# Performance work log

Measured on AMD Instinct MI355X. Metric: run time of the kernel, lower is better.

Reference implementation:

```python
import jax, jax.numpy as jnp
import numpy as np

NUM_HEADS = 32
NUM_KV_HEADS = 8  # num_heads // 4 (GQA)
HEAD_DIM = 64     # hidden_size // num_heads
ROPE_BASE = 10000.0


def _rotate_half(x):
    x1, x2 = jnp.split(x, 2, axis=-1)
    return jnp.concatenate((-x2, x1), axis=-1)


def _rope_cos_sin(seq_len, dtype):
    inv_freq = 1.0 / (ROPE_BASE ** (jnp.arange(0, HEAD_DIM, 2, dtype=jnp.float32) / HEAD_DIM))
    t = jnp.arange(seq_len, dtype=jnp.float32)
    freqs = jnp.outer(t, inv_freq)                 # [S, HEAD_DIM//2]
    emb = jnp.concatenate((freqs, freqs), axis=-1) # [S, HEAD_DIM]
    return jnp.cos(emb).astype(dtype), jnp.sin(emb).astype(dtype)


def setup_inputs() -> dict:
    key = jax.random.key(0)
    ks = jax.random.split(key, 5)
    B, S, H = 1, 2048, 2048
    KV = NUM_KV_HEADS * HEAD_DIM  # 512
    s = 0.02
    return {
        "hidden_states": jax.random.normal(ks[0], (B, S, H), jnp.float32),
        "Wq": jax.random.normal(ks[1], (H, H), jnp.float32) * s,
        "Wk": jax.random.normal(ks[2], (KV, H), jnp.float32) * s,
        "Wv": jax.random.normal(ks[3], (KV, H), jnp.float32) * s,
        "Wo": jax.random.normal(ks[4], (H, H), jnp.float32) * s,
    }


def reference(hidden_states, Wq, Wk, Wv, Wo):
    B, S, H = hidden_states.shape
    dtype = hidden_states.dtype
    # QKV projections (nn.Linear with weight [out,in], no bias)
    q = jnp.einsum("bsh,oh->bso", hidden_states, Wq)
    k = jnp.einsum("bsh,oh->bso", hidden_states, Wk)
    v = jnp.einsum("bsh,oh->bso", hidden_states, Wv)
    q = q.reshape(B, S, NUM_HEADS, HEAD_DIM).transpose(0, 2, 1, 3)      # [B,H,S,D]
    k = k.reshape(B, S, NUM_KV_HEADS, HEAD_DIM).transpose(0, 2, 1, 3)   # [B,KV,S,D]
    v = v.reshape(B, S, NUM_KV_HEADS, HEAD_DIM).transpose(0, 2, 1, 3)
    # RoPE
    cos, sin = _rope_cos_sin(S, dtype)  # [S,D] broadcast over batch/heads
    q = q * cos + _rotate_half(q) * sin
    k = k * cos + _rotate_half(k) * sin
    # GQA: repeat_interleave KV heads
    groups = NUM_HEADS // NUM_KV_HEADS
    k = jnp.repeat(k, groups, axis=1)
    v = jnp.repeat(v, groups, axis=1)
    # Attention: scores in fp32 softmax, causal mask (additive)
    scale = 1.0 / np.sqrt(HEAD_DIM)
    scores = jnp.einsum("bhqd,bhkd->bhqk", q, k) * scale
    causal = jnp.tril(jnp.ones((S, S), dtype=bool))
    scores = jnp.where(causal, scores, jnp.finfo(jnp.float32).min)
    probs = jax.nn.softmax(scores.astype(jnp.float32), axis=-1).astype(dtype)
    attn = jnp.einsum("bhqk,bhkd->bhqd", probs, v)
    attn = attn.transpose(0, 2, 1, 3).reshape(B, S, H)
    return jnp.einsum("bsh,oh->bso", attn, Wo)
```

## Files before the change

### kernel.cpp

```cpp
#include <hip/hip_runtime.h>
#include <hip/hip_bf16.h>
#include <math.h>

typedef __hip_bfloat16 bf16;
typedef __attribute__((ext_vector_type(8))) short short8;
typedef __attribute__((ext_vector_type(4))) short short4v;
typedef __attribute__((ext_vector_type(4))) float floatx4;

#define MFMA16(a, b, c) __builtin_amdgcn_mfma_f32_16x16x32_bf16((a), (b), (c), 0, 0, 0)

typedef const __attribute__((address_space(1))) void* as1_cvp;
typedef __attribute__((address_space(3))) void* as3_vp;

__device__ __forceinline__ void gload_lds16(const bf16* g, bf16* lds_uni) {
    __builtin_amdgcn_global_load_lds((as1_cvp)g, (as3_vp)lds_uni, 16, 0, 0);
}

__global__ __launch_bounds__(256) void cvt_all(
    const float* __restrict__ a0, const float* __restrict__ a1,
    const float* __restrict__ a2, const float* __restrict__ a3,
    const float* __restrict__ a4,
    bf16* __restrict__ d0, bf16* __restrict__ d1, bf16* __restrict__ d2,
    bf16* __restrict__ d3, bf16* __restrict__ d4)
{
    const int b = blockIdx.x;
    const float* src; bf16* dst; int off;
    if (b < 2048)      { src = a0; dst = d0; off = b; }
    else if (b < 4096) { src = a1; dst = d1; off = b - 2048; }
    else if (b < 4608) { src = a2; dst = d2; off = b - 4096; }
    else if (b < 5120) { src = a3; dst = d3; off = b - 4608; }
    else               { src = a4; dst = d4; off = b - 5120; }
    const int i = (off * 256 + threadIdx.x) * 8;
    const float4 x = *(const float4*)(src + i);
    const float4 y = *(const float4*)(src + i + 4);
    bf16 t[8];
    t[0] = __float2bfloat16(x.x); t[1] = __float2bfloat16(x.y);
    t[2] = __float2bfloat16(x.z); t[3] = __float2bfloat16(x.w);
    t[4] = __float2bfloat16(y.x); t[5] = __float2bfloat16(y.y);
    t[6] = __float2bfloat16(y.z); t[7] = __float2bfloat16(y.w);
    *(short8*)(dst + i) = *(const short8*)t;
}

#define GEMM_K_LOOP_12864(KB)                                                   \
    for (int k0 = 0; k0 < (KB); k0 += 64) {                                     \
        gload_lds16(gA + k0,            ldsA);                                  \
        gload_lds16(gA + A64 + k0,      ldsA + 2048);                           \
        gload_lds16(gB + k0,            ldsB);                                  \
        gload_lds16(gA + k0 + 32,       ldsA + 4096);                           \
        gload_lds16(gA + A64 + k0 + 32, ldsA + 6144);                           \
        gload_lds16(gB + k0 + 32,       ldsB + 2048);                           \
        __syncthreads();                                                        \
        _Pragma("unroll")                                                       \
        for (int hh = 0; hh < 2; ++hh) {                                        \
            short8 af[2], bfr[4];                                               \
            _Pragma("unroll")                                                   \
            for (int i = 0; i < 2; ++i)                                         \
                af[i] = *(const short8*)&As[hh * 4096 + (w * 32 + i * 16 + l15) * 32 + quad * 8]; \
            _Pragma("unroll")                                                   \
            for (int j = 0; j < 4; ++j)                                         \
                bfr[j] = *(const short8*)&Bs[hh * 2048 + (j * 16 + l15) * 32 + quad * 8]; \
            _Pragma("unroll")                                                   \
            for (int i = 0; i < 2; ++i)                                         \
                _Pragma("unroll")                                               \
                for (int j = 0; j < 4; ++j)                                     \
                    acc[i][j] = MFMA16(af[i], bfr[j], acc[i][j]);               \
        }                                                                       \
        __syncthreads();                                                        \
    }

__global__ __launch_bounds__(256) void gemm_qkv(
    const bf16* __restrict__ A, const bf16* __restrict__ Wq,
    const bf16* __restrict__ Wk, const bf16* __restrict__ Wv,
    bf16* __restrict__ qb, bf16* __restrict__ kb, bf16* __restrict__ vt)
{
    constexpr int LDK = 2048;
    __shared__ bf16 As[2 * 128 * 32];
    __shared__ bf16 Bs[2 * 64 * 32];

    const int tid  = threadIdx.x;
    const int lane = tid & 63;
    const int w    = tid >> 6;
    const int quad = lane >> 4, l15 = lane & 15;
    const int bx = blockIdx.x, by = blockIdx.y;

    const bf16* Bp; int bxl, mode;
    if (bx < 32)      { Bp = Wq; bxl = bx;      mode = 0; }
    else if (bx < 40) { Bp = Wk; bxl = bx - 32; mode = 1; }
    else              { Bp = Wv; bxl = bx - 40; mode = 2; }

    floatx4 acc[2][4];
#pragma unroll
    for (int i = 0; i < 2; ++i)
#pragma unroll
        for (int j = 0; j < 4; ++j) {
            floatx4 z = {0.f, 0.f, 0.f, 0.f};
            acc[i][j] = z;
        }

    const int srow = tid >> 2;
    const int sch  = (tid & 3) * 8;
    const bf16* gA = A  + (size_t)(by * 128 + srow) * LDK + sch;
    const bf16* gB = Bp + (size_t)(bxl * 64 + srow) * LDK + sch;
    const size_t A64 = (size_t)64 * LDK;
    bf16* ldsA = As + w * 512;
    bf16* ldsB = Bs + w * 512;

    GEMM_K_LOOP_12864(LDK)

    if (mode == 2) {
#pragma unroll
        for (int i = 0; i < 2; ++i)
#pragma unroll
            for (int j = 0; j < 4; ++j) {
                const int col = bxl * 64 + j * 16 + l15;
                const int rowb = by * 128 + w * 32 + i * 16 + quad * 4;
                bf16 t[4];
#pragma unroll
                for (int r = 0; r < 4; ++r) t[r] = __float2bfloat16(acc[i][j][r]);
                *(short4v*)&vt[(size_t)col * 2048 + rowb] = *(const short4v*)t;
            }
    } else {
        bf16* C = (mode == 0) ? qb : kb;
        const int Nn = (mode == 0) ? 2048 : 512;
        const float scale = (mode == 0) ? 0.125f : 1.0f;
        const float LOG2_1E4 = 13.28771237954945f;
        const float ifr0 = exp2f(-((float)l15) * (LOG2_1E4 / 32.f));
        const float ifr1 = exp2f(-((float)(16 + l15)) * (LOG2_1E4 / 32.f));
#pragma unroll
        for (int i = 0; i < 2; ++i) {
#pragma unroll
            for (int r = 0; r < 4; ++r) {
                const int row = by * 128 + w * 32 + i * 16 + quad * 4 + r;
                float s0, c0, s1, c1;
                sincosf((float)row * ifr0, &s0, &c0);
                sincosf((float)row * ifr1, &s1, &c1);
#pragma unroll
                for (int j = 0; j < 4; ++j) {
                    const float x  = acc[i][j][r];
                    const float xp = acc[i][j ^ 2][r];
                    const float cs = (j & 1) ? c1 : c0;
                    const float sn = (j & 1) ? s1 : s0;
                    const float oo = (x * cs + ((j < 2) ? -xp : xp) * sn) * scale;
                    const int col = bxl * 64 + j * 16 + l15;
                    C[(size_t)row * Nn + col] = __float2bfloat16(oo);
                }
            }
        }
    }
}

__global__ __launch_bounds__(256) void gemm_out(
    const bf16* __restrict__ A, const bf16* __restrict__ B, float* __restrict__ C)
{
    constexpr int LDK = 2048;
    __shared__ bf16 As[2 * 128 * 32];
    __shared__ bf16 Bs[2 * 64 * 32];

    const int tid  = threadIdx.x;
    const int lane = tid & 63;
    const int w    = tid >> 6;
    const int quad = lane >> 4, l15 = lane & 15;
    const int bx = blockIdx.x, by = blockIdx.y;

    floatx4 acc[2][4];
#pragma unroll
    for (int i = 0; i < 2; ++i)
#pragma unroll
        for (int j = 0; j < 4; ++j) {
            floatx4 z = {0.f, 0.f, 0.f, 0.f};
            acc[i][j] = z;
        }

    const int srow = tid >> 2;
    const int sch  = (tid & 3) * 8;
    const bf16* gA = A + (size_t)(by * 128 + srow) * LDK + sch;
    const bf16* gB = B + (size_t)(bx * 64 + srow) * LDK + sch;
    const size_t A64 = (size_t)64 * LDK;
    bf16* ldsA = As + w * 512;
    bf16* ldsB = Bs + w * 512;

    GEMM_K_LOOP_12864(LDK)

#pragma unroll
    for (int i = 0; i < 2; ++i)
#pragma unroll
        for (int j = 0; j < 4; ++j)
#pragma unroll
            for (int r = 0; r < 4; ++r) {
                const int row = by * 128 + w * 32 + i * 16 + quad * 4 + r;
                const int col = bx * 64 + j * 16 + l15;
                C[(size_t)row * 2048 + col] = acc[i][j][r];
            }
}

__global__ __launch_bounds__(256) void fattn4b(
    const bf16* __restrict__ q, const bf16* __restrict__ k,
    const bf16* __restrict__ vt, bf16* __restrict__ o)
{
    __shared__ bf16 Ks[2][64 * 72];
    __shared__ bf16 Vs[2][64 * 72];
    __shared__ bf16 Ps[4][16 * 68];

    const int tpair = blockIdx.x;
    const int h = blockIdx.y;
    const int kvh = h >> 2;
    const int tid = threadIdx.x, lane = tid & 63, w = tid >> 6;
    const int quad = lane >> 4, l15 = lane & 15;
    bf16* P = Ps[w];

    short ob[8];
#pragma unroll
    for (int e = 0; e < 8; ++e) ob[e] = (short)0x3F80;
    const short8 ones = *(const short8*)ob;

    const int srow = tid >> 3;
    const int ch8  = (tid & 7) * 8;
    const bf16* kg = k  + (size_t)kvh * 64 + ch8;
    const bf16* vg = vt + (size_t)(kvh * 64 + srow) * 2048 + ch8;

#pragma unroll 1
    for (int ph = 0; ph < 2; ++ph) {
        const int a = ph ? (31 - tpair) : tpair;
        const int qrow0 = a * 64 + w * 16;

        short8 qf[2];
#pragma unroll
        for (int ks = 0; ks < 2; ++ks)
            qf[ks] = *(const short8*)&q[(size_t)(qrow0 + l15) * 2048 + h * 64 + ks * 32 + quad * 8];

        floatx4 o_acc[4], l_acc;
#pragma unroll
        for (int n4 = 0; n4 < 4; ++n4) {
            floatx4 z = {0.f, 0.f, 0.f, 0.f};
            o_acc[n4] = z;
        }
        { floatx4 z = {0.f, 0.f, 0.f, 0.f}; l_acc = z; }

        {
            short8 k0 = *(const short8*)(kg + (size_t)srow * 512);
            short8 k1 = *(const short8*)(kg + (size_t)(srow + 32) * 512);
            short8 v0 = *(const short8*)(vg);
            short8 v1 = *(const short8*)(vg + (size_t)32 * 2048);
            *(short8*)&Ks[0][srow * 72 + ch8]        = k0;
            *(short8*)&Ks[0][(srow + 32) * 72 + ch8] = k1;
            *(short8*)&Vs[0][srow * 72 + ch8]        = v0;
            *(short8*)&Vs[0][(srow + 32) * 72 + ch8] = v1;
        }
        __syncthreads();

        for (int kt = 0; kt <= a; ++kt) {
            const int buf = kt & 1;

            short8 nk0, nk1, nv0, nv1;
            if (kt < a) {
                const size_t kr = (size_t)((kt + 1) * 64) * 512;
                nk0 = *(const short8*)(kg + kr + (size_t)srow * 512);
                nk1 = *(const short8*)(kg + kr + (size_t)(srow + 32) * 512);
                nv0 = *(const short8*)(vg + (kt + 1) * 64);
                nv1 = *(const short8*)(vg + (size_t)32 * 2048 + (kt + 1) * 64);
            }

            floatx4 s_acc[4];
#pragma unroll
            for (int n = 0; n < 4; ++n) {
                floatx4 z = {0.f, 0.f, 0.f, 0.f};
                s_acc[n] = z;
            }
#pragma unroll
            for (int n = 0; n < 4; ++n)
#pragma unroll
                for (int ks = 0; ks < 2; ++ks) {
                    const short8 kf = *(const short8*)&Ks[buf][(n * 16 + l15) * 72 + ks * 32 + quad * 8];
                    s_acc[n] = MFMA16(kf, qf[ks], s_acc[n]);
                }

            if (kt < a) {
#pragma unroll
                for (int n = 0; n < 4; ++n) {
                    bf16 t4[4];
#pragma unroll
                    for (int r = 0; r < 4; ++r)
                        t4[r] = __float2bfloat16(__expf(s_acc[n][r]));
                    *(short4v*)&P[l15 * 68 + n * 16 + quad * 4] = *(const short4v*)t4;
                }
            } else {
#pragma unroll
                for (int n = 0; n < 4; ++n) {
                    bf16 t4[4];
#pragma unroll
                    for (int r = 0; r < 4; ++r) {
                        const bool okc = (n * 16 + quad * 4 + r) <= (w * 16 + l15);
                        t4[r] = __float2bfloat16(okc ? __expf(s_acc[n][r]) : 0.f);
                    }
                    *(short4v*)&P[l15 * 68 + n * 16 + quad * 4] = *(const short4v*)t4;
                }
            }

#pragma unroll
            for (int ks2 = 0; ks2 < 2; ++ks2) {
                const short8 pf = *(const short8*)&P[l15 * 68 + ks2 * 32 + quad * 8];
                l_acc = MFMA16(pf, ones, l_acc);
#pragma unroll
                for (int n4 = 0; n4 < 4; ++n4) {
                    const short8 vf = *(const short8*)&Vs[buf][(n4 * 16 + l15) * 72 + ks2 * 32 + quad * 8];
                    o_acc[n4] = MFMA16(pf, vf, o_acc[n4]);
                }
            }

            if (kt < a) {
                *(short8*)&Ks[buf ^ 1][srow * 72 + ch8]        = nk0;
                *(short8*)&Ks[buf ^ 1][(srow + 32) * 72 + ch8] = nk1;
                *(short8*)&Vs[buf ^ 1][srow * 72 + ch8]        = nv0;
                *(short8*)&Vs[buf ^ 1][(srow + 32) * 72 + ch8] = nv1;
            }
            __syncthreads();
        }

#pragma unroll
        for (int n4 = 0; n4 < 4; ++n4)
#pragma unroll
            for (int r = 0; r < 4; ++r) {
                const float val = o_acc[n4][r] / l_acc[r];
                const int row = qrow0 + quad * 4 + r;
                const int col = h * 64 + n4 * 16 + l15;
                o[(size_t)row * 2048 + col] = __float2bfloat16(val);
            }
    }
}

extern "C" void kernel_launch(void* const* d_in, const int* in_sizes, int n_in,
                              void* d_out, int out_size, void* d_ws, size_t ws_size,
                              hipStream_t stream)
{
    const float* hs = (const float*)d_in[0];
    const float* Wq = (const float*)d_in[1];
    const float* Wk = (const float*)d_in[2];
    const float* Wv = (const float*)d_in[3];
    const float* Wo = (const float*)d_in[4];
    float* out = (float*)d_out;

    bf16* ws  = (bf16*)d_ws;
    bf16* hsb = ws;
    bf16* Wqb = ws + 4194304;
    bf16* Wkb = ws + 8388608;
    bf16* Wvb = ws + 9437184;
    bf16* Wob = ws + 10485760;
    bf16* qb  = ws + 14680064;
    bf16* kb  = ws + 18874368;
    bf16* vtb = ws + 19922944;
    bf16* ab  = ws + 20971520;

    dim3 blk(256);
    cvt_all<<<7168, blk, 0, stream>>>(hs, Wq, Wk, Wv, Wo, hsb, Wqb, Wkb, Wvb, Wob);
    gemm_qkv<<<dim3(48, 16), blk, 0, stream>>>(hsb, Wqb, Wkb, Wvb, qb, kb, vtb);
    fattn4b<<<dim3(16, 32), blk, 0, stream>>>(qb, kb, vtb, ab);
    gemm_out<<<dim3(32, 16), blk, 0, stream>>>(ab, Wob, out);
}
```

Before: 223.3 us.

## Double-buffer LDS tiles in QKV and output GEMM K loops

Both GEMM kernels now hold two LDS stages and issue the global-to-LDS loads for the next K tile before computing on the current one. Explicit vmcnt waits and raw s_barrier calls replace __syncthreads, so load latency can overlap the MFMA work. This doubles LDS use per block (48KB), which may reduce occupancy, and it relies on hand-placed waitcnt for correctness.

```diff
diff --git a/kernel.cpp b/kernel.cpp
--- a/kernel.cpp
+++ b/kernel.cpp
@@ -41,31 +41,48 @@
     *(short8*)(dst + i) = *(const short8*)t;
 }
 
-#define GEMM_K_LOOP_12864(KB)                                                   \
-    for (int k0 = 0; k0 < (KB); k0 += 64) {                                     \
-        gload_lds16(gA + k0,            ldsA);                                  \
-        gload_lds16(gA + A64 + k0,      ldsA + 2048);                           \
-        gload_lds16(gB + k0,            ldsB);                                  \
-        gload_lds16(gA + k0 + 32,       ldsA + 4096);                           \
-        gload_lds16(gA + A64 + k0 + 32, ldsA + 6144);                           \
-        gload_lds16(gB + k0 + 32,       ldsB + 2048);                           \
-        __syncthreads();                                                        \
-        _Pragma("unroll")                                                       \
-        for (int hh = 0; hh < 2; ++hh) {                                        \
-            short8 af[2], bfr[4];                                               \
+#define GEMM_STAGE6(k0, sA, sB)                                                 \
+    gload_lds16(gA + (k0),            (sA));                                    \
+    gload_lds16(gA + A64 + (k0),      (sA) + 2048);                             \
+    gload_lds16(gB + (k0),            (sB));                                    \
+    gload_lds16(gA + (k0) + 32,       (sA) + 4096);                             \
+    gload_lds16(gA + A64 + (k0) + 32, (sA) + 6144);                             \
+    gload_lds16(gB + (k0) + 32,       (sB) + 2048);
+
+#define GEMM_K_LOOP_DB(KB)                                                      \
+    {                                                                           \
+        bf16* sA0 = &As[0][0] + w * 512; bf16* sB0 = &Bs[0][0] + w * 512;       \
+        bf16* sA1 = &As[1][0] + w * 512; bf16* sB1 = &Bs[1][0] + w * 512;       \
+        GEMM_STAGE6(0, sA0, sB0)                                                \
+        for (int k0 = 0; k0 < (KB); k0 += 64) {                                 \
+            const int cur = (k0 >> 6) & 1;                                      \
+            if (k0 + 64 < (KB)) {                                               \
+                if (cur == 0) { GEMM_STAGE6(k0 + 64, sA1, sB1) }                \
+                else          { GEMM_STAGE6(k0 + 64, sA0, sB0) }                \
+                asm volatile("s_waitcnt vmcnt(6)" ::: "memory");                \
+            } else {                                                            \
+                asm volatile("s_waitcnt vmcnt(0)" ::: "memory");                \
+            }                                                                   \
+            __builtin_amdgcn_s_barrier();                                       \
+            const bf16* Acur = &As[cur][0];                                     \
+            const bf16* Bcur = &Bs[cur][0];                                     \
             _Pragma("unroll")                                                   \
-            for (int i = 0; i < 2; ++i)                                         \
-                af[i] = *(const short8*)&As[hh * 4096 + (w * 32 + i * 16 + l15) * 32 + quad * 8]; \
-            _Pragma("unroll")                                                   \
-            for (int j = 0; j < 4; ++j)                                         \
-                bfr[j] = *(const short8*)&Bs[hh * 2048 + (j * 16 + l15) * 32 + quad * 8]; \
-            _Pragma("unroll")                                                   \
-            for (int i = 0; i < 2; ++i)                                         \
+            for (int hh = 0; hh < 2; ++hh) {                                    \
+                short8 af[2], bfr[4];                                           \
+                _Pragma("unroll")                                               \
+                for (int i = 0; i < 2; ++i)                                     \
+                    af[i] = *(const short8*)&Acur[hh * 4096 + (w * 32 + i * 16 + l15) * 32 + quad * 8]; \
                 _Pragma("unroll")                                               \
                 for (int j = 0; j < 4; ++j)                                     \
-                    acc[i][j] = MFMA16(af[i], bfr[j], acc[i][j]);               \
+                    bfr[j] = *(const short8*)&Bcur[hh * 2048 + (j * 16 + l15) * 32 + quad * 8]; \
+                _Pragma("unroll")                                               \
+                for (int i = 0; i < 2; ++i)                                     \
+                    _Pragma("unroll")                                           \
+                    for (int j = 0; j < 4; ++j)                                 \
+                        acc[i][j] = MFMA16(af[i], bfr[j], acc[i][j]);           \
+            }                                                                   \
+            __builtin_amdgcn_s_barrier();                                       \
         }                                                                       \
-        __syncthreads();                                                        \
     }
 
 __global__ __launch_bounds__(256) void gemm_qkv(
@@ -74,8 +91,8 @@
     bf16* __restrict__ qb, bf16* __restrict__ kb, bf16* __restrict__ vt)
 {
     constexpr int LDK = 2048;
-    __shared__ bf16 As[2 * 128 * 32];
-    __shared__ bf16 Bs[2 * 64 * 32];
+    __shared__ bf16 As[2][128 * 64];
+    __shared__ bf16 Bs[2][64 * 64];
 
     const int tid  = threadIdx.x;
     const int lane = tid & 63;
@@ -102,10 +119,8 @@
     const bf16* gA = A  + (size_t)(by * 128 + srow) * LDK + sch;
     const bf16* gB = Bp + (size_t)(bxl * 64 + srow) * LDK + sch;
     const size_t A64 = (size_t)64 * LDK;
-    bf16* ldsA = As + w * 512;
-    bf16* ldsB = Bs + w * 512;
-
-    GEMM_K_LOOP_12864(LDK)
+
+    GEMM_K_LOOP_DB(LDK)
 
     if (mode == 2) {
 #pragma unroll
@@ -153,8 +168,8 @@
     const bf16* __restrict__ A, const bf16* __restrict__ B, float* __restrict__ C)
 {
     constexpr int LDK = 2048;
-    __shared__ bf16 As[2 * 128 * 32];
-    __shared__ bf16 Bs[2 * 64 * 32];
+    __shared__ bf16 As[2][128 * 64];
+    __shared__ bf16 Bs[2][64 * 64];
 
     const int tid  = threadIdx.x;
     const int lane = tid & 63;
@@ -176,10 +191,8 @@
     const bf16* gA = A + (size_t)(by * 128 + srow) * LDK + sch;
     const bf16* gB = B + (size_t)(bx * 64 + srow) * LDK + sch;
     const size_t A64 = (size_t)64 * LDK;
-    bf16* ldsA = As + w * 512;
-    bf16* ldsB = Bs + w * 512;
-
-    GEMM_K_LOOP_12864(LDK)
+
+    GEMM_K_LOOP_DB(LDK)
 
 #pragma unroll
     for (int i = 0; i < 2; ++i)
```

After: 219.6 us. About the same (-1.7%).
